# Kernel tuning notes

Hardware: AMD Instinct MI355X
Metric: run time of the kernel (lower is better)

The kernel has to match this reference:

```python
import jax, jax.numpy as jnp
import numpy as np

B = 256      # graph pairs
N = 256      # nodes per graph (uniform -> padding is a reshape)
DEG = 16     # avg degree
D = 32       # one_hot_dim
F1, F2, F3 = 128, 64, 64
T = 16       # tensor_neurons
BINS = 16
BOT = 16     # bottle_neck_neurons


def setup_inputs() -> dict:
    key = jax.random.key(0)
    ks = jax.random.split(key, 24)
    NT = B * N            # total nodes per side
    NE = B * N * DEG      # total directed edges per side
    x_q = jax.random.normal(ks[0], (NT, D), jnp.float32)
    x_c = jax.random.normal(ks[1], (NT, D), jnp.float32)
    edge_q = jax.random.randint(ks[2], (2, NE), 0, NT, jnp.int32)
    edge_c = jax.random.randint(ks[3], (2, NE), 0, NT, jnp.int32)
    qgraph_sizes = jnp.full((B,), N, jnp.int32)
    cgraph_sizes = jnp.full((B,), N, jnp.int32)

    def glorot(k, shape):
        fan = sum(shape[-2:]) if len(shape) >= 2 else shape[0] * 2
        return jax.random.uniform(k, shape, jnp.float32, -1.0, 1.0) * np.sqrt(6.0 / fan)

    params = dict(
        W1=glorot(ks[4], (D, F1)), b1=jnp.zeros((F1,), jnp.float32),
        W2=glorot(ks[5], (F1, F2)), b2=jnp.zeros((F2,), jnp.float32),
        W3=glorot(ks[6], (F2, F3)), b3=jnp.zeros((F3,), jnp.float32),
        attn_w=glorot(ks[7], (F3, F3)),
        ntn_a_w=glorot(ks[8], (T, F3, F3)),
        ntn_b_w=glorot(ks[9], (2 * F3, T)),
        ntn_bias=glorot(ks[10], (T, 1)),
        fc1_w=glorot(ks[11], (T + BINS, BOT)), fc1_b=jnp.zeros((BOT,), jnp.float32),
        fc2_w=glorot(ks[12], (BOT, 1)), fc2_b=jnp.zeros((1,), jnp.float32),
    )
    return dict(x_q=x_q, edge_q=edge_q, x_c=x_c, edge_c=edge_c,
                qgraph_sizes=qgraph_sizes, cgraph_sizes=cgraph_sizes, **params)


def _gcn(x, src, dst, W, b):
    n = x.shape[0]
    h = x @ W
    loop = jnp.arange(n, dtype=src.dtype)
    s = jnp.concatenate([src, loop])
    d = jnp.concatenate([dst, loop])
    deg = jax.ops.segment_sum(jnp.ones(s.shape, h.dtype), d, num_segments=n)
    dinv = jnp.where(deg > 0, jax.lax.rsqrt(jnp.maximum(deg, 1.0)), 0.0)
    coef = (dinv[s] * dinv[d])[:, None]
    return jax.ops.segment_sum(h[s] * coef, d, num_segments=n) + b


def _gnn(x, ei, W1, b1, W2, b2, W3, b3):
    src, dst = ei[0], ei[1]
    h = jax.nn.relu(_gcn(x, src, dst, W1, b1))        # dropout is identity in eval
    h = jax.nn.relu(_gcn(h, src, dst, W2, b2))
    return _gcn(h, src, dst, W3, b3)                  # [B*N, F3]


def _att_pool(q, attn_w, sizes):
    # q: [B, N, F3]
    ctx = jnp.tanh((q.sum(axis=1) @ attn_w) / sizes.astype(q.dtype)[:, None])  # [B, F3]
    sig = jax.nn.sigmoid(jnp.einsum('bnf,bf->bn', q, ctx))                      # [B, N]
    return jnp.einsum('bnf,bn->bf', q, sig)                                     # [B, F3]


def _pair_hist(q, c):
    # per-pair histogram of q @ c^T with BINS bins over each pair's [min, max]
    s = jax.lax.stop_gradient(jnp.einsum('bnf,bmf->bnm', q, c))  # [B, N, N]
    mn = s.min(axis=(1, 2), keepdims=True)
    mx = s.max(axis=(1, 2), keepdims=True)
    idx = jnp.clip(jnp.floor((s - mn) / jnp.maximum(mx - mn, 1e-12) * BINS),
                   0, BINS - 1).astype(jnp.int32)
    gid = (idx + jnp.arange(B, dtype=jnp.int32)[:, None, None] * BINS).reshape(-1)
    h = jax.ops.segment_sum(jnp.ones(gid.shape, jnp.float32), gid,
                            num_segments=B * BINS).reshape(B, BINS)
    return h / h.sum(axis=1, keepdims=True)


def reference(x_q, edge_q, x_c, edge_c, qgraph_sizes, cgraph_sizes,
              W1, b1, W2, b2, W3, b3, attn_w, ntn_a_w, ntn_b_w, ntn_bias,
              fc1_w, fc1_b, fc2_w, fc2_b):
    q = _gnn(x_q, edge_q, W1, b1, W2, b2, W3, b3).reshape(B, N, F3)
    c = _gnn(x_c, edge_c, W1, b1, W2, b2, W3, b3).reshape(B, N, F3)
    e1 = _att_pool(q, attn_w, qgraph_sizes)
    e2 = _att_pool(c, attn_w, cgraph_sizes)
    ntn = (jnp.einsum('bi,tij,bj->bt', e1, ntn_a_w, e2)
           + jnp.concatenate([e1, e2], axis=-1) @ ntn_b_w
           + ntn_bias[:, 0])
    scores = jax.nn.relu(ntn)                                   # [B, T]
    hist = _pair_hist(q, c)                                     # [B, BINS]
    scores = jnp.concatenate([scores, hist], axis=1)
    scores = jax.nn.relu(scores @ fc1_w + fc1_b)
    p = jax.nn.sigmoid(scores @ fc2_w + fc2_b)[:, 0]            # [B]
    ged = -0.5 * (qgraph_sizes + cgraph_sizes).astype(p.dtype) * jnp.log(p)
    return ged
```

## Files before the change

### kernel.cpp

```cpp
#include <hip/hip_runtime.h>
#include <hip/hip_bf16.h>
#include <math.h>

#define BB 256
#define NN 256
#define NT (BB*NN)
#define NT2 (2*NT)
#define NE (NT*16)
#define DD 32
#define F1C 128
#define F2C 64
#define F3C 64
#define TT 16
#define BINS 16

#define NBUCK 256
#define BSHIFT 9
#define BNODES 512
#define BCAP 10240
#define EPB 4096

typedef __attribute__((ext_vector_type(8))) short short8;
typedef __attribute__((ext_vector_type(4))) float f32x4;
typedef __attribute__((ext_vector_type(2))) float f32x2;

__device__ inline float b2f(ushort u) { return __uint_as_float(((uint)u) << 16); }
__device__ inline ushort f2b(float f) {
    uint u = __float_as_uint(f);
    return (ushort)((u + 0x7fffu + ((u >> 16) & 1u)) >> 16);
}
__device__ inline float clamp8(float v) { return fminf(fmaxf(v, -448.0f), 448.0f); }
__device__ inline uchar f2f8(float v) {
    int r = __builtin_amdgcn_cvt_pk_fp8_f32(clamp8(v), 0.0f, 0, false);
    return (uchar)(r & 0xff);
}
__device__ inline void f8x8_acc(uint2 w, float* acc) {
    f32x2 p;
    p = __builtin_amdgcn_cvt_pk_f32_fp8(w.x, false); acc[0] += p.x; acc[1] += p.y;
    p = __builtin_amdgcn_cvt_pk_f32_fp8(w.x, true);  acc[2] += p.x; acc[3] += p.y;
    p = __builtin_amdgcn_cvt_pk_f32_fp8(w.y, false); acc[4] += p.x; acc[5] += p.y;
    p = __builtin_amdgcn_cvt_pk_f32_fp8(w.y, true);  acc[6] += p.x; acc[7] += p.y;
}
__device__ inline uint2 f8x8_pack(const float* v) {
    uint2 r;
    r.x = (uint)__builtin_amdgcn_cvt_pk_fp8_f32(clamp8(v[0]), clamp8(v[1]), 0, false);
    r.x = (uint)__builtin_amdgcn_cvt_pk_fp8_f32(clamp8(v[2]), clamp8(v[3]), (int)r.x, true);
    r.y = (uint)__builtin_amdgcn_cvt_pk_fp8_f32(clamp8(v[4]), clamp8(v[5]), 0, false);
    r.y = (uint)__builtin_amdgcn_cvt_pk_fp8_f32(clamp8(v[6]), clamp8(v[7]), (int)r.y, true);
    return r;
}

__global__ __launch_bounds__(256) void zero_k(int* __restrict__ gcount) {
    gcount[threadIdx.x] = 0;
}

__global__ __launch_bounds__(256) void csr_p1_k(const int* __restrict__ eq, const int* __restrict__ ec,
                                                uint* __restrict__ staged, int* __restrict__ gcount) {
    __shared__ uint s_pk[EPB];
    __shared__ int s_cnt[NBUCK];
    __shared__ int s_off[NBUCK];
    __shared__ int s_base[NBUCK];
    __shared__ int s_gb[NBUCK];
    int t = threadIdx.x;
    bool sideB = blockIdx.x >= 256;
    const int* edge = sideB ? ec : eq;
    int off = sideB ? NT : 0;
    int e0 = (blockIdx.x & 255) * EPB;
    s_cnt[t] = 0;
    __syncthreads();
    uint pk[16]; int bk[16];
#pragma unroll
    for (int j = 0; j < 16; j++) {
        int e = e0 + j * 256 + t;
        int s = edge[e] + off;
        int d = edge[NE + e] + off;
        bk[j] = d >> BSHIFT;
        pk[j] = ((uint)s << BSHIFT) | (uint)(d & (BNODES - 1));
        atomicAdd(&s_cnt[bk[j]], 1);
    }
    __syncthreads();
    s_off[t] = s_cnt[t];
    __syncthreads();
    for (int o = 1; o < NBUCK; o <<= 1) {
        int x = (t >= o) ? s_off[t - o] : 0;
        __syncthreads();
        s_off[t] += x;
        __syncthreads();
    }
    {
        int ex = s_off[t] - s_cnt[t];
        s_base[t] = ex;
        s_off[t] = ex;
        s_gb[t] = atomicAdd(&gcount[t], s_cnt[t]);
    }
    __syncthreads();
#pragma unroll
    for (int j = 0; j < 16; j++) {
        int pos = atomicAdd(&s_off[bk[j]], 1);
        s_pk[pos] = pk[j];
    }
    __syncthreads();
    int w = t >> 6, l = t & 63;
    int bsel = l >> 4, l16 = l & 15;
    for (int pb = w; pb < NBUCK / 4; pb += 4) {
        int b = pb * 4 + bsel;
        int n = s_cnt[b], st = s_base[b], gb = s_gb[b];
        if (gb + n > BCAP) n = max(0, BCAP - gb);
        for (int i = l16; i < n; i += 16)
            staged[b * BCAP + gb + i] = s_pk[st + i];
    }
}

__global__ __launch_bounds__(256) void csr_p2_k(const uint* __restrict__ staged, const int* __restrict__ gcount,
                                                int* __restrict__ rp, int* __restrict__ indeg,
                                                float* __restrict__ dinv, int* __restrict__ ep) {
    int b = blockIdx.x;
    int t = threadIdx.x;
    __shared__ int cnt[BNODES];
    __shared__ int fl[BNODES];
    __shared__ int wsum[256];
    __shared__ int gsc[NBUCK];
    cnt[t] = 0; cnt[t + 256] = 0;
    gsc[t] = min(gcount[t], BCAP);
    __syncthreads();
    for (int off = 1; off < NBUCK; off <<= 1) {
        int x = (t >= off) ? gsc[t - off] : 0;
        __syncthreads();
        gsc[t] += x;
        __syncthreads();
    }
    int gbase = (b == 0) ? 0 : gsc[b - 1];
    int n = min(gcount[b], BCAP);
    const uint* sb = staged + (size_t)b * BCAP;
    int i = t;
    for (; i + 768 < n; i += 1024) {
        uint p0 = sb[i];
        uint p1 = sb[i + 256];
        uint p2 = sb[i + 512];
        uint p3 = sb[i + 768];
        atomicAdd(&cnt[p0 & (BNODES - 1)], 1);
        atomicAdd(&cnt[p1 & (BNODES - 1)], 1);
        atomicAdd(&cnt[p2 & (BNODES - 1)], 1);
        atomicAdd(&cnt[p3 & (BNODES - 1)], 1);
    }
    for (; i < n; i += 256)
        atomicAdd(&cnt[sb[i] & (BNODES - 1)], 1);
    __syncthreads();
    int base2 = t * 2;
    int c0 = cnt[base2], c1 = cnt[base2 + 1];
    int s2 = c0 + c1;
    wsum[t] = s2;
    __syncthreads();
    for (int off = 1; off < 256; off <<= 1) {
        int x = (t >= off) ? wsum[t - off] : 0;
        __syncthreads();
        wsum[t] += x;
        __syncthreads();
    }
    int p = gbase + wsum[t] - s2;
    int v0 = b * BNODES + base2;
    rp[v0] = p;          fl[base2] = p;
    indeg[v0] = c0;      dinv[v0] = rsqrtf((float)(c0 + 1));
    p += c0;
    rp[v0 + 1] = p;      fl[base2 + 1] = p;
    indeg[v0 + 1] = c1;  dinv[v0 + 1] = rsqrtf((float)(c1 + 1));
    __syncthreads();
    i = t;
    for (; i + 768 < n; i += 1024) {
        uint p0 = sb[i];
        uint p1 = sb[i + 256];
        uint p2 = sb[i + 512];
        uint p3 = sb[i + 768];
        ep[atomicAdd(&fl[p0 & (BNODES - 1)], 1)] = (int)(p0 >> BSHIFT);
        ep[atomicAdd(&fl[p1 & (BNODES - 1)], 1)] = (int)(p1 >> BSHIFT);
        ep[atomicAdd(&fl[p2 & (BNODES - 1)], 1)] = (int)(p2 >> BSHIFT);
        ep[atomicAdd(&fl[p3 & (BNODES - 1)], 1)] = (int)(p3 >> BSHIFT);
    }
    for (; i < n; i += 256) {
        uint pk = sb[i];
        ep[atomicAdd(&fl[pk & (BNODES - 1)], 1)] = (int)(pk >> BSHIFT);
    }
}

__global__ __launch_bounds__(256) void cvt2w_k(const float* __restrict__ a, const float* __restrict__ b,
                                               const float* __restrict__ dinv, ushort* __restrict__ out,
                                               const float* __restrict__ W1, const float* __restrict__ W2,
                                               const float* __restrict__ W3, ushort* __restrict__ Wt1,
                                               ushort* __restrict__ Wt2, uchar* __restrict__ Wt3f8) {
    const int NB_X = NT2 * DD / 4 / 256;
    if (blockIdx.x < NB_X) {
        int i = blockIdx.x * 256 + threadIdx.x;
        const int per = NT * DD / 4;
        bool sideB = i >= per;
        const float4* src = (const float4*)(sideB ? b : a);
        float4 v = src[sideB ? i - per : i];
        float dv = dinv[i / (DD / 4)];
        ushort4 o;
        o.x = f2b(v.x * dv); o.y = f2b(v.y * dv); o.z = f2b(v.z * dv); o.w = f2b(v.w * dv);
        ((ushort4*)out)[i] = o;
    } else {
        int i = (blockIdx.x - NB_X) * 256 + threadIdx.x;
        if (i < DD * F1C)  { int k = i / F1C, n = i % F1C; Wt1[n * DD + k]  = f2b(W1[i]); }
        if (i < F1C * F2C) { int k = i / F2C, n = i % F2C; Wt2[n * F1C + k] = f2b(W2[i]); }
        if (i < F2C * F3C) { int k = i / F3C, n = i % F3C; Wt3f8[n * F2C + k] = f2f8(W3[i]); }
    }
}

template<int F, bool BIAS, bool RELU>
__global__ __launch_bounds__(256) void agg_bf_k(const ushort* __restrict__ in, const int* __restrict__ rp,
                                                const int* __restrict__ indeg, const int* __restrict__ ep,
                                                const float* __restrict__ dinv,
                                                const float* __restrict__ bias, ushort* __restrict__ out) {
    constexpr int LPV = F / 8;
    constexpr int VPB = 256 / LPV;
    int g = threadIdx.x / LPV;
    int l = threadIdx.x % LPV;
    int v = blockIdx.x * VPB + g;
    float dv = dinv[v];
    short8 rs = *(const short8*)(in + (size_t)v * F + l * 8);
    float acc[8];
#pragma unroll
    for (int j = 0; j < 8; j++) acc[j] = b2f((ushort)rs[j]);
    int start = rp[v];
    int cnt   = indeg[v];
    int i = 0;
    for (; i + 4 <= cnt; i += 4) {
        int s0 = ep[start + i];
        int s1 = ep[start + i + 1];
        int s2 = ep[start + i + 2];
        int s3 = ep[start + i + 3];
        short8 r0 = *(const short8*)(in + (size_t)s0 * F + l * 8);
        short8 r1 = *(const short8*)(in + (size_t)s1 * F + l * 8);
        short8 r2 = *(const short8*)(in + (size_t)s2 * F + l * 8);
        short8 r3 = *(const short8*)(in + (size_t)s3 * F + l * 8);
#pragma unroll
        for (int j = 0; j < 8; j++) {
            acc[j] += b2f((ushort)r0[j]);
            acc[j] += b2f((ushort)r1[j]);
            acc[j] += b2f((ushort)r2[j]);
            acc[j] += b2f((ushort)r3[j]);
        }
    }
    for (; i < cnt; i++) {
        int s0 = ep[start + i];
        short8 r0 = *(const short8*)(in + (size_t)s0 * F + l * 8);
#pragma unroll
        for (int j = 0; j < 8; j++) acc[j] += b2f((ushort)r0[j]);
    }
    short8 o;
#pragma unroll
    for (int j = 0; j < 8; j++) {
        float x = dv * acc[j];
        if (BIAS) x += bias[l * 8 + j];
        if (RELU) x = fmaxf(x, 0.0f);
        o[j] = (short)f2b(x);
    }
    *(short8*)(out + (size_t)v * F + l * 8) = o;
}

template<bool OUT_BF16, bool BIAS, bool RELU>
__global__ __launch_bounds__(256) void agg_f8_k(const uchar* __restrict__ in, const int* __restrict__ rp,
                                                const int* __restrict__ indeg, const int* __restrict__ ep,
                                                const float* __restrict__ dinv,
                                                const float* __restrict__ bias, void* __restrict__ outp) {
    int g = threadIdx.x >> 3;
    int l = threadIdx.x & 7;
    int v = blockIdx.x * 32 + g;
    float dv = dinv[v];
    float acc[8] = {0, 0, 0, 0, 0, 0, 0, 0};
    f8x8_acc(*(const uint2*)(in + (size_t)v * 64 + l * 8), acc);
    int start = rp[v];
    int cnt   = indeg[v];
    int i = 0;
    for (; i + 8 <= cnt; i += 8) {
        int sx[8];
#pragma unroll
        for (int j = 0; j < 8; j++) sx[j] = ep[start + i + j];
        uint2 gx[8];
#pragma unroll
        for (int j = 0; j < 8; j++) gx[j] = *(const uint2*)(in + (size_t)sx[j] * 64 + l * 8);
#pragma unroll
        for (int j = 0; j < 8; j++) f8x8_acc(gx[j], acc);
    }
    for (; i + 4 <= cnt; i += 4) {
        int s0 = ep[start + i];
        int s1 = ep[start + i + 1];
        int s2 = ep[start + i + 2];
        int s3 = ep[start + i + 3];
        uint2 g0 = *(const uint2*)(in + (size_t)s0 * 64 + l * 8);
        uint2 g1 = *(const uint2*)(in + (size_t)s1 * 64 + l * 8);
        uint2 g2 = *(const uint2*)(in + (size_t)s2 * 64 + l * 8);
        uint2 g3 = *(const uint2*)(in + (size_t)s3 * 64 + l * 8);
        f8x8_acc(g0, acc); f8x8_acc(g1, acc); f8x8_acc(g2, acc); f8x8_acc(g3, acc);
    }
    for (; i < cnt; i++) {
        int s0 = ep[start + i];
        f8x8_acc(*(const uint2*)(in + (size_t)s0 * 64 + l * 8), acc);
    }
#pragma unroll
    for (int j = 0; j < 8; j++) {
        float x = dv * acc[j];
        if (BIAS) x += bias[l * 8 + j];
        if (RELU) x = fmaxf(x, 0.0f);
        acc[j] = x;
    }
    if (OUT_BF16) {
        short8 o;
#pragma unroll
        for (int j = 0; j < 8; j++) o[j] = (short)f2b(acc[j]);
        *(short8*)((ushort*)outp + (size_t)v * 64 + l * 8) = o;
    } else {
        *(uint2*)((uchar*)outp + (size_t)v * 64 + l * 8) = f8x8_pack(acc);
    }
}

__global__ __launch_bounds__(256) void gemm12_k(const ushort* __restrict__ xa,
                                                const ushort* __restrict__ Wt1,
                                                const float* __restrict__ b1,
                                                const ushort* __restrict__ Wt2,
                                                const float* __restrict__ dinv,
                                                uchar* __restrict__ h8a) {
    __shared__ ushort s_h1[128][136];
    int w = threadIdx.x >> 6, lane = threadIdx.x & 63;
    int r16 = lane & 15, quad = lane >> 4, koff = quad * 8;
    size_t rows0 = (size_t)blockIdx.x * 128;

    short8 af1[2];
#pragma unroll
    for (int mt = 0; mt < 2; mt++)
        af1[mt] = *(const short8*)(xa + (rows0 + (w * 2 + mt) * 16 + r16) * 32 + koff);
#pragma unroll
    for (int nt = 0; nt < 8; nt++) {
        short8 bfr = *(const short8*)(Wt1 + (size_t)(nt * 16 + r16) * 32 + koff);
        f32x4 acc[2] = {{0.f,0.f,0.f,0.f},{0.f,0.f,0.f,0.f}};
        acc[0] = __builtin_amdgcn_mfma_f32_16x16x32_bf16(af1[0], bfr, acc[0], 0, 0, 0);
        acc[1] = __builtin_amdgcn_mfma_f32_16x16x32_bf16(af1[1], bfr, acc[1], 0, 0, 0);
        int col = nt * 16 + r16;
        float bc = b1[col];
#pragma unroll
        for (int mt = 0; mt < 2; mt++)
#pragma unroll
            for (int r = 0; r < 4; r++) {
                int rl = (w * 2 + mt) * 16 + quad * 4 + r;
                s_h1[rl][col] = f2b(fmaxf(acc[mt][r] + bc, 0.0f));
            }
    }
    __syncthreads();

    short8 af2[4][2];
#pragma unroll
    for (int kc = 0; kc < 4; kc++)
#pragma unroll
        for (int mt = 0; mt < 2; mt++)
            af2[kc][mt] = *(const short8*)&s_h1[(w * 2 + mt) * 16 + r16][kc * 32 + koff];
    float dvr[2][4];
#pragma unroll
    for (int mt = 0; mt < 2; mt++)
#pragma unroll
        for (int r = 0; r < 4; r++)
            dvr[mt][r] = dinv[rows0 + (w * 2 + mt) * 16 + quad * 4 + r];
#pragma unroll
    for (int nt = 0; nt < 4; nt++) {
        f32x4 acc[2] = {{0.f,0.f,0.f,0.f},{0.f,0.f,0.f,0.f}};
#pragma unroll
        for (int kc = 0; kc < 4; kc++) {
            short8 bfr = *(const short8*)(Wt2 + (size_t)(nt * 16 + r16) * 128 + kc * 32 + koff);
            acc[0] = __builtin_amdgcn_mfma_f32_16x16x32_bf16(af2[kc][0], bfr, acc[0], 0, 0, 0);
            acc[1] = __builtin_amdgcn_mfma_f32_16x16x32_bf16(af2[kc][1], bfr, acc[1], 0, 0, 0);
        }
#pragma unroll
        for (int mt = 0; mt < 2; mt++)
#pragma unroll
            for (int r = 0; r < 4; r++) {
                size_t row = rows0 + (w * 2 + mt) * 16 + quad * 4 + r;
                int col = nt * 16 + r16;
                h8a[row * 64 + col] = f2f8(acc[mt][r] * dvr[mt][r]);
            }
    }
}

__global__ __launch_bounds__(256) void gemm_f8_k(const uchar* __restrict__ A8,
                                                 const uchar* __restrict__ Wt8,
                                                 const float* __restrict__ dinv,
                                                 uchar* __restrict__ out8) {
    int w = threadIdx.x >> 6, lane = threadIdx.x & 63;
    int r16 = lane & 15, koff = (lane >> 4) * 8;
    size_t rows0 = (size_t)blockIdx.x * 128;

    long af[2][2];
#pragma unroll
    for (int kc = 0; kc < 2; kc++)
#pragma unroll
        for (int mt = 0; mt < 2; mt++)
            af[kc][mt] = *(const long*)(A8 + (rows0 + (w * 2 + mt) * 16 + r16) * 64 + kc * 32 + koff);

    float dvr[2][4];
#pragma unroll
    for (int mt = 0; mt < 2; mt++)
#pragma unroll
        for (int r = 0; r < 4; r++)
            dvr[mt][r] = dinv[rows0 + (w * 2 + mt) * 16 + (lane >> 4) * 4 + r];

#pragma unroll
    for (int nt = 0; nt < 4; nt++) {
        f32x4 acc[2] = {{0.f,0.f,0.f,0.f},{0.f,0.f,0.f,0.f}};
#pragma unroll
        for (int kc = 0; kc < 2; kc++) {
            long b = *(const long*)(Wt8 + (size_t)(nt * 16 + r16) * 64 + kc * 32 + koff);
            acc[0] = __builtin_amdgcn_mfma_f32_16x16x32_fp8_fp8(af[kc][0], b, acc[0], 0, 0, 0);
            acc[1] = __builtin_amdgcn_mfma_f32_16x16x32_fp8_fp8(af[kc][1], b, acc[1], 0, 0, 0);
        }
#pragma unroll
        for (int mt = 0; mt < 2; mt++) {
#pragma unroll
            for (int r = 0; r < 4; r++) {
                size_t row = rows0 + (w * 2 + mt) * 16 + (lane >> 4) * 4 + r;
                int col = nt * 16 + (lane & 15);
                out8[row * 64 + col] = f2f8(acc[mt][r] * dvr[mt][r]);
            }
        }
    }
}

__global__ __launch_bounds__(256) void pool_hist_k(const ushort* __restrict__ fin,
                                                   const int* __restrict__ qsz, const int* __restrict__ csz,
                                                   const float* __restrict__ attn_w,
                                                   float* __restrict__ e_out, float* __restrict__ histp) {
    __shared__ float smemf[17472];
    int t = threadIdx.x;
    if (blockIdx.x < 512) {
        int b = blockIdx.x & 255;
        bool is_c = blockIdx.x >= BB;
        const ushort* emb = fin + (size_t)blockIdx.x * NN * F3C;
        float size = (float)((is_c ? csz : qsz)[b]);
        float* eo = e_out + (is_c ? BB * F3C : 0) + b * F3C;
        float (*s_emb)[F3C + 1] = (float(*)[F3C + 1])smemf;
        float* s_red = smemf + 256 * 65;
        float* s_sq  = s_red + 256;
        float* s_ctx = s_sq + 64;
        float* s_sig = s_ctx + 64;
        int f = t & 63;
        int w = t >> 6;
#pragma unroll
        for (int it = 0; it < 8; it++) {
            int idx = it * 2048 + t * 8;
            int row = idx >> 6, f0 = idx & 63;
            short8 v = *(const short8*)(emb + idx);
#pragma unroll
            for (int j = 0; j < 8; j++) s_emb[row][f0 + j] = b2f((ushort)v[j]);
        }
        __syncthreads();
        float psum = 0.0f;
#pragma unroll 8
        for (int i2 = 0; i2 < 64; i2++) psum += s_emb[w * 64 + i2][f];
        s_red[w * 64 + f] = psum;
        __syncthreads();
        if (w == 0) {
            s_sq[f] = s_red[f] + s_red[64 + f] + s_red[128 + f] + s_red[192 + f];
            float acc = 0.0f;
            for (int k = 0; k < 64; k++) acc += s_sq[k] * attn_w[k * 64 + f];
            s_ctx[f] = tanhf(acc / size);
        }
        __syncthreads();
        {
            float acc = 0.0f;
#pragma unroll 8
            for (int k = 0; k < 64; k++) acc += s_emb[t][k] * s_ctx[k];
            s_sig[t] = 1.0f / (1.0f + expf(-acc));
        }
        __syncthreads();
        float eacc = 0.0f;
#pragma unroll 8
        for (int i = 0; i < 64; i++) {
            int n = w * 64 + i;
            eacc += s_sig[n] * s_emb[n][f];
        }
        s_red[w * 64 + f] = eacc;
        __syncthreads();
        if (w == 0) eo[f] = s_red[f] + s_red[64 + f] + s_red[128 + f] + s_red[192 + f];
    } else {
        int b = blockIdx.x - 512;
        const ushort* qb = fin + (size_t)b * NN * 64;
        const ushort* cb = fin + (size_t)(NT + b * NN) * 64;
        int lane = t & 63;
        int w = t >> 6;
        int r16 = lane & 15, koff = (lane >> 4) * 8;
        ushort (*cb_s)[72] = (ushort(*)[72])smemf;
        int* h = (int*)(smemf + 9216);
        int* hp = h + 16 * 256;
        float* smn = (float*)(hp + 256);
        float* smx = smn + 4;
        float* s_sc = smx + 4;

#pragma unroll
        for (int it = 0; it < 8; it++) {
            int idx = it * 2048 + t * 8;
            int row = idx >> 6, f0 = idx & 63;
            *(short8*)&cb_s[row][f0] = *(const short8*)(cb + idx);
        }
        short8 a[4][2];
#pragma unroll
        for (int i = 0; i < 4; i++) {
            int row = (w * 4 + i) * 16 + r16;
#pragma unroll
            for (int kk = 0; kk < 2; kk++)
                a[i][kk] = *(const short8*)(qb + row * 64 + kk * 32 + koff);
        }
        __syncthreads();
        float mn = 1e30f, mx = -1e30f;
        for (int mt = 0; mt < 16; mt++) {
            int crow = mt * 16 + r16;
            short8 b0 = *(const short8*)&cb_s[crow][koff];
            short8 b1 = *(const short8*)&cb_s[crow][32 + koff];
#pragma unroll
            for (int i = 0; i < 4; i++) {
                f32x4 acc = {0.0f, 0.0f, 0.0f, 0.0f};
                acc = __builtin_amdgcn_mfma_f32_16x16x32_bf16(a[i][0], b0, acc, 0, 0, 0);
                acc = __builtin_amdgcn_mfma_f32_16x16x32_bf16(a[i][1], b1, acc, 0, 0, 0);
                mn = fminf(mn, fminf(fminf(acc[0], acc[1]), fminf(acc[2], acc[3])));
                mx = fmaxf(mx, fmaxf(fmaxf(acc[0], acc[1]), fmaxf(acc[2], acc[3])));
            }
        }
        for (int off = 32; off; off >>= 1) {
            mn = fminf(mn, __shfl_xor(mn, off, 64));
            mx = fmaxf(mx, __shfl_xor(mx, off, 64));
        }
        if (lane == 0) { smn[w] = mn; smx[w] = mx; }
        __syncthreads();
        if (t == 0) {
            float m0 = fminf(fminf(smn[0], smn[1]), fminf(smn[2], smn[3]));
            float m1 = fmaxf(fmaxf(smx[0], smx[1]), fmaxf(smx[2], smx[3]));
            s_sc[0] = m0;
            s_sc[1] = 16.0f / fmaxf(m1 - m0, 1e-12f);
        }
#pragma unroll
        for (int i = 0; i < 16; i++) h[i * 256 + t] = 0;
        __syncthreads();
        float bmn = s_sc[0], bscale = s_sc[1];
        for (int mt = 0; mt < 16; mt++) {
            int crow = mt * 16 + r16;
            short8 b0 = *(const short8*)&cb_s[crow][koff];
            short8 b1 = *(const short8*)&cb_s[crow][32 + koff];
#pragma unroll
            for (int i = 0; i < 4; i++) {
                f32x4 acc = {0.0f, 0.0f, 0.0f, 0.0f};
                acc = __builtin_amdgcn_mfma_f32_16x16x32_bf16(a[i][0], b0, acc, 0, 0, 0);
                acc = __builtin_amdgcn_mfma_f32_16x16x32_bf16(a[i][1], b1, acc, 0, 0, 0);
#pragma unroll
                for (int r = 0; r < 4; r++) {
                    int bin = (int)floorf((acc[r] - bmn) * bscale);
                    bin = min(max(bin, 0), 15);
                    h[bin * 256 + t] += 1;
                }
            }
        }
        __syncthreads();
        int bb = t >> 4, part = t & 15;
        int sum = 0;
#pragma unroll
        for (int j = 0; j < 16; j++) sum += h[bb * 256 + part * 16 + j];
        hp[bb * 16 + part] = sum;
        __syncthreads();
        if (t < 16) {
            int s = 0;
#pragma unroll
            for (int j = 0; j < 16; j++) s += hp[t * 16 + j];
            histp[b * 16 + t] = (float)s;
        }
    }
}

__global__ __launch_bounds__(256) void ntn_final_k(const float* __restrict__ e, const float* __restrict__ A,
                                                   const float* __restrict__ bw, const float* __restrict__ bias,
                                                   const float* __restrict__ histp,
                                                   const float* __restrict__ fc1w, const float* __restrict__ fc1b,
                                                   const float* __restrict__ fc2w, const float* __restrict__ fc2b,
                                                   const int* __restrict__ qsz, const int* __restrict__ csz,
                                                   float* __restrict__ out) {
    int b = blockIdx.x;
    int t = threadIdx.x;
    __shared__ float s_e1[64], s_e2[64];
    __shared__ float s_ntn[16];
    __shared__ float s_s[32];
    __shared__ float s_a[16];
    if (t < 64) s_e1[t] = e[b * 64 + t];
    else if (t < 128) s_e2[t - 64] = e[BB * 64 + b * 64 + (t - 64)];
    if (t < 16) s_ntn[t] = 0.0f;
    __syncthreads();
#pragma unroll
    for (int r = 0; r < 4; r++) {
        int idx = t + r * 256;
        int tt = idx >> 6, i = idx & 63;
        const float* Ar = A + (size_t)idx * 64;
        float acc = 0.0f;
        for (int j = 0; j < 64; j++) acc += Ar[j] * s_e2[j];
        atomicAdd(&s_ntn[tt], s_e1[i] * acc);
    }
    __syncthreads();
    if (t < 16) {
        float acc = s_ntn[t] + bias[t];
        for (int k = 0; k < 64; k++) acc += s_e1[k] * bw[k * 16 + t];
        for (int k = 0; k < 64; k++) acc += s_e2[k] * bw[(64 + k) * 16 + t];
        s_s[t] = fmaxf(acc, 0.0f);
        s_s[16 + t] = histp[b * 16 + t] * (1.0f / 65536.0f);
    }
    __syncthreads();
    if (t < 16) {
        float a = fc1b[t];
        for (int k = 0; k < 32; k++) a += s_s[k] * fc1w[k * 16 + t];
        s_a[t] = fmaxf(a, 0.0f);
    }
    __syncthreads();
    if (t == 0) {
        float z = fc2b[0];
        for (int j = 0; j < 16; j++) z += s_a[j] * fc2w[j];
        float nz = -z;
        float sp = (nz > 20.0f) ? nz : log1pf(expf(nz));
        out[b] = 0.5f * (float)(qsz[b] + csz[b]) * sp;
    }
}

extern "C" void kernel_launch(void* const* d_in, const int* in_sizes, int n_in,
                              void* d_out, int out_size, void* d_ws, size_t ws_size,
                              hipStream_t stream) {
    const float* x_q    = (const float*)d_in[0];
    const int*   edge_q = (const int*)d_in[1];
    const float* x_c    = (const float*)d_in[2];
    const int*   edge_c = (const int*)d_in[3];
    const int*   qsz    = (const int*)d_in[4];
    const int*   csz    = (const int*)d_in[5];
    const float* W1 = (const float*)d_in[6];
    const float* b1 = (const float*)d_in[7];
    const float* W2 = (const float*)d_in[8];
    const float* b2 = (const float*)d_in[9];
    const float* W3 = (const float*)d_in[10];
    const float* b3 = (const float*)d_in[11];
    const float* attn_w  = (const float*)d_in[12];
    const float* ntn_a   = (const float*)d_in[13];
    const float* ntn_b   = (const float*)d_in[14];
    const float* ntn_bias= (const float*)d_in[15];
    const float* fc1w = (const float*)d_in[16];
    const float* fc1b = (const float*)d_in[17];
    const float* fc2w = (const float*)d_in[18];
    const float* fc2b = (const float*)d_in[19];
    float* out = (float*)d_out;

    char* w = (char*)d_ws;
    auto alloc = [&](size_t bytes) -> void* {
        void* p = (void*)w;
        w += (bytes + 255) & ~(size_t)255;
        return p;
    };
    int*    rp     = (int*)alloc((size_t)NT2 * 4);
    int*    indeg  = (int*)alloc((size_t)NT2 * 4);
    float*  dinv   = (float*)alloc((size_t)NT2 * 4);
    int*    gcount = (int*)alloc(NBUCK * 4);
    uint*   staged = (uint*)alloc((size_t)NBUCK * BCAP * 4);
    int*    ep     = (int*)alloc((size_t)2 * NE * 4);
    ushort* xb     = (ushort*)alloc((size_t)NT2 * 32 * 2);
    ushort* xa     = (ushort*)alloc((size_t)NT2 * 32 * 2);
    uchar*  h8a    = (uchar*)alloc((size_t)NT2 * 64);
    uchar*  h8b    = (uchar*)alloc((size_t)NT2 * 64);
    ushort* fin    = (ushort*)alloc((size_t)NT2 * 64 * 2);
    ushort* Wt1    = (ushort*)alloc((size_t)DD * F1C * 2);
    ushort* Wt2    = (ushort*)alloc((size_t)F1C * F2C * 2);
    uchar*  Wt3f8  = (uchar*)alloc((size_t)F2C * F3C);
    float*  e12    = (float*)alloc(2 * BB * 64 * 4);
    float*  histp  = (float*)alloc(256 * 16 * 4);

    zero_k<<<1, 256, 0, stream>>>(gcount);
    csr_p1_k<<<512, 256, 0, stream>>>(edge_q, edge_c, staged, gcount);
    csr_p2_k<<<NBUCK, 256, 0, stream>>>(staged, gcount, rp, indeg, dinv, ep);

    cvt2w_k<<<NT2 * 32 / 4 / 256 + 64, 256, 0, stream>>>(x_q, x_c, dinv, xb,
                                                         W1, W2, W3, Wt1, Wt2, Wt3f8);

    agg_bf_k<32, false, false><<<NT2 / 64, 256, 0, stream>>>(xb, rp, indeg, ep, dinv, nullptr, xa);
    gemm12_k<<<NT2 / 128, 256, 0, stream>>>(xa, Wt1, b1, Wt2, dinv, h8a);
    agg_f8_k<false, true, true><<<NT2 / 32, 256, 0, stream>>>(h8a, rp, indeg, ep, dinv, b2, h8b);
    gemm_f8_k<<<NT2 / 128, 256, 0, stream>>>(h8b, Wt3f8, dinv, h8a);
    agg_f8_k<true, true, false><<<NT2 / 32, 256, 0, stream>>>(h8a, rp, indeg, ep, dinv, b3, fin);

    pool_hist_k<<<768, 256, 0, stream>>>(fin, qsz, csz, attn_w, e12, histp);
    ntn_final_k<<<BB, 256, 0, stream>>>(e12, ntn_a, ntn_b, ntn_bias, histp,
                                        fc1w, fc1b, fc2w, fc2b, qsz, csz, out);
}
```

Before: 285.5 us.

## Fuse neighbor aggregation into GEMM kernels and merge CSR pass with input conversion

Aggregation for layers 1 and 2 now runs inside the same kernel as the following dense transform, with the aggregated rows staged in LDS instead of written to and reread from global memory. Input conversion no longer waits on dinv, so it is folded into the CSR bucketing kernel and source-side dinv is applied per edge during the gather. The NTN kernel replaces LDS atomics with vectorized loads and a wave shuffle reduction. Together these cut launches and intermediate traffic, at the cost of extra per-edge dinv loads and fewer, heavier blocks for the gather phase.

```diff
diff --git a/kernel.cpp b/kernel.cpp
--- a/kernel.cpp
+++ b/kernel.cpp
@@ -54,60 +54,81 @@
     gcount[threadIdx.x] = 0;
 }
 
-__global__ __launch_bounds__(256) void csr_p1_k(const int* __restrict__ eq, const int* __restrict__ ec,
-                                                uint* __restrict__ staged, int* __restrict__ gcount) {
-    __shared__ uint s_pk[EPB];
-    __shared__ int s_cnt[NBUCK];
-    __shared__ int s_off[NBUCK];
-    __shared__ int s_base[NBUCK];
-    __shared__ int s_gb[NBUCK];
+__global__ __launch_bounds__(256) void p1cvt_k(const int* __restrict__ eq, const int* __restrict__ ec,
+                                               uint* __restrict__ staged, int* __restrict__ gcount,
+                                               const float* __restrict__ a, const float* __restrict__ b,
+                                               ushort* __restrict__ out,
+                                               const float* __restrict__ W1, const float* __restrict__ W2,
+                                               const float* __restrict__ W3, ushort* __restrict__ Wt1,
+                                               ushort* __restrict__ Wt2, uchar* __restrict__ Wt3f8) {
     int t = threadIdx.x;
-    bool sideB = blockIdx.x >= 256;
-    const int* edge = sideB ? ec : eq;
-    int off = sideB ? NT : 0;
-    int e0 = (blockIdx.x & 255) * EPB;
-    s_cnt[t] = 0;
-    __syncthreads();
-    uint pk[16]; int bk[16];
-#pragma unroll
-    for (int j = 0; j < 16; j++) {
-        int e = e0 + j * 256 + t;
-        int s = edge[e] + off;
-        int d = edge[NE + e] + off;
-        bk[j] = d >> BSHIFT;
-        pk[j] = ((uint)s << BSHIFT) | (uint)(d & (BNODES - 1));
-        atomicAdd(&s_cnt[bk[j]], 1);
-    }
-    __syncthreads();
-    s_off[t] = s_cnt[t];
-    __syncthreads();
-    for (int o = 1; o < NBUCK; o <<= 1) {
-        int x = (t >= o) ? s_off[t - o] : 0;
-        __syncthreads();
-        s_off[t] += x;
-        __syncthreads();
-    }
-    {
-        int ex = s_off[t] - s_cnt[t];
-        s_base[t] = ex;
-        s_off[t] = ex;
-        s_gb[t] = atomicAdd(&gcount[t], s_cnt[t]);
-    }
-    __syncthreads();
-#pragma unroll
-    for (int j = 0; j < 16; j++) {
-        int pos = atomicAdd(&s_off[bk[j]], 1);
-        s_pk[pos] = pk[j];
-    }
-    __syncthreads();
-    int w = t >> 6, l = t & 63;
-    int bsel = l >> 4, l16 = l & 15;
-    for (int pb = w; pb < NBUCK / 4; pb += 4) {
-        int b = pb * 4 + bsel;
-        int n = s_cnt[b], st = s_base[b], gb = s_gb[b];
-        if (gb + n > BCAP) n = max(0, BCAP - gb);
-        for (int i = l16; i < n; i += 16)
-            staged[b * BCAP + gb + i] = s_pk[st + i];
+    if (blockIdx.x < 512) {
+        __shared__ uint s_pk[EPB];
+        __shared__ int s_cnt[NBUCK];
+        __shared__ int s_off[NBUCK];
+        __shared__ int s_base[NBUCK];
+        __shared__ int s_gb[NBUCK];
+        bool sideB = blockIdx.x >= 256;
+        const int* edge = sideB ? ec : eq;
+        int off = sideB ? NT : 0;
+        int e0 = (blockIdx.x & 255) * EPB;
+        s_cnt[t] = 0;
+        __syncthreads();
+        uint pk[16]; int bk[16];
+#pragma unroll
+        for (int j = 0; j < 16; j++) {
+            int e = e0 + j * 256 + t;
+            int s = edge[e] + off;
+            int d = edge[NE + e] + off;
+            bk[j] = d >> BSHIFT;
+            pk[j] = ((uint)s << BSHIFT) | (uint)(d & (BNODES - 1));
+            atomicAdd(&s_cnt[bk[j]], 1);
+        }
+        __syncthreads();
+        s_off[t] = s_cnt[t];
+        __syncthreads();
+        for (int o = 1; o < NBUCK; o <<= 1) {
+            int x = (t >= o) ? s_off[t - o] : 0;
+            __syncthreads();
+            s_off[t] += x;
+            __syncthreads();
+        }
+        {
+            int ex = s_off[t] - s_cnt[t];
+            s_base[t] = ex;
+            s_off[t] = ex;
+            s_gb[t] = atomicAdd(&gcount[t], s_cnt[t]);
+        }
+        __syncthreads();
+#pragma unroll
+        for (int j = 0; j < 16; j++) {
+            int pos = atomicAdd(&s_off[bk[j]], 1);
+            s_pk[pos] = pk[j];
+        }
+        __syncthreads();
+        int w = t >> 6, l = t & 63;
+        int bsel = l >> 4, l16 = l & 15;
+        for (int pb = w; pb < NBUCK / 4; pb += 4) {
+            int bkt = pb * 4 + bsel;
+            int n = s_cnt[bkt], st = s_base[bkt], gb = s_gb[bkt];
+            if (gb + n > BCAP) n = max(0, BCAP - gb);
+            for (int i = l16; i < n; i += 16)
+                staged[bkt * BCAP + gb + i] = s_pk[st + i];
+        }
+    } else if (blockIdx.x < 512 + NT2 * DD / 4 / 256) {
+        int i = (blockIdx.x - 512) * 256 + t;
+        const int per = NT * DD / 4;
+        bool sideB = i >= per;
+        const float4* src = (const float4*)(sideB ? b : a);
+        float4 v = src[sideB ? i - per : i];
+        ushort4 o;
+        o.x = f2b(v.x); o.y = f2b(v.y); o.z = f2b(v.z); o.w = f2b(v.w);
+        ((ushort4*)out)[i] = o;
+    } else {
+        int i = (blockIdx.x - (512 + NT2 * DD / 4 / 256)) * 256 + t;
+        if (i < DD * F1C)  { int k = i / F1C, n = i % F1C; Wt1[n * DD + k]  = f2b(W1[i]); }
+        if (i < F1C * F2C) { int k = i / F2C, n = i % F2C; Wt2[n * F1C + k] = f2b(W2[i]); }
+        if (i < F2C * F3C) { int k = i / F3C, n = i % F3C; Wt3f8[n * F2C + k] = f2f8(W3[i]); }
     }
 }
 
@@ -182,80 +203,201 @@
     }
 }
 
-__global__ __launch_bounds__(256) void cvt2w_k(const float* __restrict__ a, const float* __restrict__ b,
-                                               const float* __restrict__ dinv, ushort* __restrict__ out,
-                                               const float* __restrict__ W1, const float* __restrict__ W2,
-                                               const float* __restrict__ W3, ushort* __restrict__ Wt1,
-                                               ushort* __restrict__ Wt2, uchar* __restrict__ Wt3f8) {
-    const int NB_X = NT2 * DD / 4 / 256;
-    if (blockIdx.x < NB_X) {
-        int i = blockIdx.x * 256 + threadIdx.x;
-        const int per = NT * DD / 4;
-        bool sideB = i >= per;
-        const float4* src = (const float4*)(sideB ? b : a);
-        float4 v = src[sideB ? i - per : i];
-        float dv = dinv[i / (DD / 4)];
-        ushort4 o;
-        o.x = f2b(v.x * dv); o.y = f2b(v.y * dv); o.z = f2b(v.z * dv); o.w = f2b(v.w * dv);
-        ((ushort4*)out)[i] = o;
-    } else {
-        int i = (blockIdx.x - NB_X) * 256 + threadIdx.x;
-        if (i < DD * F1C)  { int k = i / F1C, n = i % F1C; Wt1[n * DD + k]  = f2b(W1[i]); }
-        if (i < F1C * F2C) { int k = i / F2C, n = i % F2C; Wt2[n * F1C + k] = f2b(W2[i]); }
-        if (i < F2C * F3C) { int k = i / F3C, n = i % F3C; Wt3f8[n * F2C + k] = f2f8(W3[i]); }
-    }
-}
-
-template<int F, bool BIAS, bool RELU>
-__global__ __launch_bounds__(256) void agg_bf_k(const ushort* __restrict__ in, const int* __restrict__ rp,
-                                                const int* __restrict__ indeg, const int* __restrict__ ep,
-                                                const float* __restrict__ dinv,
-                                                const float* __restrict__ bias, ushort* __restrict__ out) {
-    constexpr int LPV = F / 8;
-    constexpr int VPB = 256 / LPV;
-    int g = threadIdx.x / LPV;
-    int l = threadIdx.x % LPV;
-    int v = blockIdx.x * VPB + g;
-    float dv = dinv[v];
-    short8 rs = *(const short8*)(in + (size_t)v * F + l * 8);
-    float acc[8];
-#pragma unroll
-    for (int j = 0; j < 8; j++) acc[j] = b2f((ushort)rs[j]);
-    int start = rp[v];
-    int cnt   = indeg[v];
-    int i = 0;
-    for (; i + 4 <= cnt; i += 4) {
-        int s0 = ep[start + i];
-        int s1 = ep[start + i + 1];
-        int s2 = ep[start + i + 2];
-        int s3 = ep[start + i + 3];
-        short8 r0 = *(const short8*)(in + (size_t)s0 * F + l * 8);
-        short8 r1 = *(const short8*)(in + (size_t)s1 * F + l * 8);
-        short8 r2 = *(const short8*)(in + (size_t)s2 * F + l * 8);
-        short8 r3 = *(const short8*)(in + (size_t)s3 * F + l * 8);
-#pragma unroll
-        for (int j = 0; j < 8; j++) {
-            acc[j] += b2f((ushort)r0[j]);
-            acc[j] += b2f((ushort)r1[j]);
-            acc[j] += b2f((ushort)r2[j]);
-            acc[j] += b2f((ushort)r3[j]);
-        }
-    }
-    for (; i < cnt; i++) {
-        int s0 = ep[start + i];
-        short8 r0 = *(const short8*)(in + (size_t)s0 * F + l * 8);
-#pragma unroll
-        for (int j = 0; j < 8; j++) acc[j] += b2f((ushort)r0[j]);
-    }
-    short8 o;
-#pragma unroll
-    for (int j = 0; j < 8; j++) {
-        float x = dv * acc[j];
-        if (BIAS) x += bias[l * 8 + j];
-        if (RELU) x = fmaxf(x, 0.0f);
-        o[j] = (short)f2b(x);
-    }
-    *(short8*)(out + (size_t)v * F + l * 8) = o;
+__global__ __launch_bounds__(256) void l1_k(const ushort* __restrict__ xb,
+                                            const ushort* __restrict__ Wt1,
+                                            const float* __restrict__ b1,
+                                            const ushort* __restrict__ Wt2,
+                                            const int* __restrict__ rp,
+                                            const int* __restrict__ indeg,
+                                            const int* __restrict__ ep,
+                                            const float* __restrict__ dinv,
+                                            uchar* __restrict__ h8a) {
+    __shared__ ushort s_x[128][40];
+    __shared__ ushort s_h1[128][136];
+    int t = threadIdx.x;
+    size_t rows0 = (size_t)blockIdx.x * 128;
+
+    int gl = t >> 2;
+    int l4 = t & 3;
+#pragma unroll
+    for (int vt = 0; vt < 2; vt++) {
+        int vloc = vt * 64 + gl;
+        int v = (int)rows0 + vloc;
+        float dv = dinv[v];
+        short8 rs = *(const short8*)(xb + (size_t)v * 32 + l4 * 8);
+        float acc[8];
+#pragma unroll
+        for (int j = 0; j < 8; j++) acc[j] = dv * b2f((ushort)rs[j]);
+        int start = rp[v];
+        int cnt   = indeg[v];
+        int i = 0;
+        for (; i + 8 <= cnt; i += 8) {
+            int sx[8];
+#pragma unroll
+            for (int j = 0; j < 8; j++) sx[j] = ep[start + i + j];
+            float ds[8];
+#pragma unroll
+            for (int j = 0; j < 8; j++) ds[j] = dinv[sx[j]];
+            short8 r[8];
+#pragma unroll
+            for (int j = 0; j < 8; j++) r[j] = *(const short8*)(xb + (size_t)sx[j] * 32 + l4 * 8);
+#pragma unroll
+            for (int j = 0; j < 8; j++)
+#pragma unroll
+                for (int k = 0; k < 8; k++) acc[k] += ds[j] * b2f((ushort)r[j][k]);
+        }
+        for (; i < cnt; i++) {
+            int s0 = ep[start + i];
+            float d0 = dinv[s0];
+            short8 r0 = *(const short8*)(xb + (size_t)s0 * 32 + l4 * 8);
+#pragma unroll
+            for (int j = 0; j < 8; j++) acc[j] += d0 * b2f((ushort)r0[j]);
+        }
+        short8 o;
+#pragma unroll
+        for (int j = 0; j < 8; j++) o[j] = (short)f2b(dv * acc[j]);
+        *(short8*)&s_x[vloc][l4 * 8] = o;
+    }
+    __syncthreads();
+
+    int w = t >> 6, lane = t & 63;
+    int r16 = lane & 15, quad = lane >> 4, koff = quad * 8;
+
+    short8 af1[2];
+#pragma unroll
+    for (int mt = 0; mt < 2; mt++)
+        af1[mt] = *(const short8*)&s_x[(w * 2 + mt) * 16 + r16][koff];
+#pragma unroll
+    for (int nt = 0; nt < 8; nt++) {
+        short8 bfr = *(const short8*)(Wt1 + (size_t)(nt * 16 + r16) * 32 + koff);
+        f32x4 acc[2] = {{0.f,0.f,0.f,0.f},{0.f,0.f,0.f,0.f}};
+        acc[0] = __builtin_amdgcn_mfma_f32_16x16x32_bf16(af1[0], bfr, acc[0], 0, 0, 0);
+        acc[1] = __builtin_amdgcn_mfma_f32_16x16x32_bf16(af1[1], bfr, acc[1], 0, 0, 0);
+        int col = nt * 16 + r16;
+        float bc = b1[col];
+#pragma unroll
+        for (int mt = 0; mt < 2; mt++)
+#pragma unroll
+            for (int r = 0; r < 4; r++) {
+                int rl = (w * 2 + mt) * 16 + quad * 4 + r;
+                s_h1[rl][col] = f2b(fmaxf(acc[mt][r] + bc, 0.0f));
+            }
+    }
+    __syncthreads();
+
+    short8 af2[4][2];
+#pragma unroll
+    for (int kc = 0; kc < 4; kc++)
+#pragma unroll
+        for (int mt = 0; mt < 2; mt++)
+            af2[kc][mt] = *(const short8*)&s_h1[(w * 2 + mt) * 16 + r16][kc * 32 + koff];
+    float dvr[2][4];
+#pragma unroll
+    for (int mt = 0; mt < 2; mt++)
+#pragma unroll
+        for (int r = 0; r < 4; r++)
+            dvr[mt][r] = dinv[rows0 + (w * 2 + mt) * 16 + quad * 4 + r];
+#pragma unroll
+    for (int nt = 0; nt < 4; nt++) {
+        f32x4 acc[2] = {{0.f,0.f,0.f,0.f},{0.f,0.f,0.f,0.f}};
+#pragma unroll
+        for (int kc = 0; kc < 4; kc++) {
+            short8 bfr = *(const short8*)(Wt2 + (size_t)(nt * 16 + r16) * 128 + kc * 32 + koff);
+            acc[0] = __builtin_amdgcn_mfma_f32_16x16x32_bf16(af2[kc][0], bfr, acc[0], 0, 0, 0);
+            acc[1] = __builtin_amdgcn_mfma_f32_16x16x32_bf16(af2[kc][1], bfr, acc[1], 0, 0, 0);
+        }
+#pragma unroll
+        for (int mt = 0; mt < 2; mt++)
+#pragma unroll
+            for (int r = 0; r < 4; r++) {
+                size_t row = rows0 + (w * 2 + mt) * 16 + quad * 4 + r;
+                int col = nt * 16 + r16;
+                h8a[row * 64 + col] = f2f8(acc[mt][r] * dvr[mt][r]);
+            }
+    }
+}
+
+__global__ __launch_bounds__(256) void l2_k(const uchar* __restrict__ in,
+                                            const int* __restrict__ rp,
+                                            const int* __restrict__ indeg,
+                                            const int* __restrict__ ep,
+                                            const float* __restrict__ dinv,
+                                            const float* __restrict__ b2,
+                                            const uchar* __restrict__ Wt8,
+                                            uchar* __restrict__ out8) {
+    __shared__ uchar s_a[128][72];
+    int t = threadIdx.x;
+    size_t rows0 = (size_t)blockIdx.x * 128;
+
+    int g8 = t >> 3;
+    int l8 = t & 7;
+#pragma unroll
+    for (int pass = 0; pass < 4; pass++) {
+        int vloc = pass * 32 + g8;
+        int v = (int)rows0 + vloc;
+        float dv = dinv[v];
+        float acc[8] = {0, 0, 0, 0, 0, 0, 0, 0};
+        f8x8_acc(*(const uint2*)(in + (size_t)v * 64 + l8 * 8), acc);
+        int start = rp[v];
+        int cnt   = indeg[v];
+        int i = 0;
+        for (; i + 8 <= cnt; i += 8) {
+            int sx[8];
+#pragma unroll
+            for (int j = 0; j < 8; j++) sx[j] = ep[start + i + j];
+            uint2 gx[8];
+#pragma unroll
+            for (int j = 0; j < 8; j++) gx[j] = *(const uint2*)(in + (size_t)sx[j] * 64 + l8 * 8);
+#pragma unroll
+            for (int j = 0; j < 8; j++) f8x8_acc(gx[j], acc);
+        }
+        for (; i < cnt; i++) {
+            int s0 = ep[start + i];
+            f8x8_acc(*(const uint2*)(in + (size_t)s0 * 64 + l8 * 8), acc);
+        }
+#pragma unroll
+        for (int j = 0; j < 8; j++)
+            acc[j] = fmaxf(dv * acc[j] + b2[l8 * 8 + j], 0.0f);
+        *(uint2*)&s_a[vloc][l8 * 8] = f8x8_pack(acc);
+    }
+    __syncthreads();
+
+    int w = t >> 6, lane = t & 63;
+    int r16 = lane & 15, koff = (lane >> 4) * 8;
+
+    long af[2][2];
+#pragma unroll
+    for (int kc = 0; kc < 2; kc++)
+#pragma unroll
+        for (int mt = 0; mt < 2; mt++)
+            af[kc][mt] = *(const long*)&s_a[(w * 2 + mt) * 16 + r16][kc * 32 + koff];
+
+    float dvr[2][4];
+#pragma unroll
+    for (int mt = 0; mt < 2; mt++)
+#pragma unroll
+        for (int r = 0; r < 4; r++)
+            dvr[mt][r] = dinv[rows0 + (w * 2 + mt) * 16 + (lane >> 4) * 4 + r];
+
+#pragma unroll
+    for (int nt = 0; nt < 4; nt++) {
+        f32x4 acc[2] = {{0.f,0.f,0.f,0.f},{0.f,0.f,0.f,0.f}};
+#pragma unroll
+        for (int kc = 0; kc < 2; kc++) {
+            long b = *(const long*)(Wt8 + (size_t)(nt * 16 + r16) * 64 + kc * 32 + koff);
+            acc[0] = __builtin_amdgcn_mfma_f32_16x16x32_fp8_fp8(af[kc][0], b, acc[0], 0, 0, 0);
+            acc[1] = __builtin_amdgcn_mfma_f32_16x16x32_fp8_fp8(af[kc][1], b, acc[1], 0, 0, 0);
+        }
+#pragma unroll
+        for (int mt = 0; mt < 2; mt++) {
+#pragma unroll
+            for (int r = 0; r < 4; r++) {
+                size_t row = rows0 + (w * 2 + mt) * 16 + (lane >> 4) * 4 + r;
+                int col = nt * 16 + (lane & 15);
+                out8[row * 64 + col] = f2f8(acc[mt][r] * dvr[mt][r]);
+            }
+        }
+    }
 }
 
 template<bool OUT_BF16, bool BIAS, bool RELU>
@@ -311,114 +453,6 @@
         *(short8*)((ushort*)outp + (size_t)v * 64 + l * 8) = o;
     } else {
         *(uint2*)((uchar*)outp + (size_t)v * 64 + l * 8) = f8x8_pack(acc);
-    }
-}
-
-__global__ __launch_bounds__(256) void gemm12_k(const ushort* __restrict__ xa,
-                                                const ushort* __restrict__ Wt1,
-                                                const float* __restrict__ b1,
-                                                const ushort* __restrict__ Wt2,
-                                                const float* __restrict__ dinv,
-                                                uchar* __restrict__ h8a) {
-    __shared__ ushort s_h1[128][136];
-    int w = threadIdx.x >> 6, lane = threadIdx.x & 63;
-    int r16 = lane & 15, quad = lane >> 4, koff = quad * 8;
-    size_t rows0 = (size_t)blockIdx.x * 128;
-
-    short8 af1[2];
-#pragma unroll
-    for (int mt = 0; mt < 2; mt++)
-        af1[mt] = *(const short8*)(xa + (rows0 + (w * 2 + mt) * 16 + r16) * 32 + koff);
-#pragma unroll
-    for (int nt = 0; nt < 8; nt++) {
-        short8 bfr = *(const short8*)(Wt1 + (size_t)(nt * 16 + r16) * 32 + koff);
-        f32x4 acc[2] = {{0.f,0.f,0.f,0.f},{0.f,0.f,0.f,0.f}};
-        acc[0] = __builtin_amdgcn_mfma_f32_16x16x32_bf16(af1[0], bfr, acc[0], 0, 0, 0);
-        acc[1] = __builtin_amdgcn_mfma_f32_16x16x32_bf16(af1[1], bfr, acc[1], 0, 0, 0);
-        int col = nt * 16 + r16;
-        float bc = b1[col];
-#pragma unroll
-        for (int mt = 0; mt < 2; mt++)
-#pragma unroll
-            for (int r = 0; r < 4; r++) {
-                int rl = (w * 2 + mt) * 16 + quad * 4 + r;
-                s_h1[rl][col] = f2b(fmaxf(acc[mt][r] + bc, 0.0f));
-            }
-    }
-    __syncthreads();
-
-    short8 af2[4][2];
-#pragma unroll
-    for (int kc = 0; kc < 4; kc++)
-#pragma unroll
-        for (int mt = 0; mt < 2; mt++)
-            af2[kc][mt] = *(const short8*)&s_h1[(w * 2 + mt) * 16 + r16][kc * 32 + koff];
-    float dvr[2][4];
-#pragma unroll
-    for (int mt = 0; mt < 2; mt++)
-#pragma unroll
-        for (int r = 0; r < 4; r++)
-            dvr[mt][r] = dinv[rows0 + (w * 2 + mt) * 16 + quad * 4 + r];
-#pragma unroll
-    for (int nt = 0; nt < 4; nt++) {
-        f32x4 acc[2] = {{0.f,0.f,0.f,0.f},{0.f,0.f,0.f,0.f}};
-#pragma unroll
-        for (int kc = 0; kc < 4; kc++) {
-            short8 bfr = *(const short8*)(Wt2 + (size_t)(nt * 16 + r16) * 128 + kc * 32 + koff);
-            acc[0] = __builtin_amdgcn_mfma_f32_16x16x32_bf16(af2[kc][0], bfr, acc[0], 0, 0, 0);
-            acc[1] = __builtin_amdgcn_mfma_f32_16x16x32_bf16(af2[kc][1], bfr, acc[1], 0, 0, 0);
-        }
-#pragma unroll
-        for (int mt = 0; mt < 2; mt++)
-#pragma unroll
-            for (int r = 0; r < 4; r++) {
-                size_t row = rows0 + (w * 2 + mt) * 16 + quad * 4 + r;
-                int col = nt * 16 + r16;
-                h8a[row * 64 + col] = f2f8(acc[mt][r] * dvr[mt][r]);
-            }
-    }
-}
-
-__global__ __launch_bounds__(256) void gemm_f8_k(const uchar* __restrict__ A8,
-                                                 const uchar* __restrict__ Wt8,
-                                                 const float* __restrict__ dinv,
-                                                 uchar* __restrict__ out8) {
-    int w = threadIdx.x >> 6, lane = threadIdx.x & 63;
-    int r16 = lane & 15, koff = (lane >> 4) * 8;
-    size_t rows0 = (size_t)blockIdx.x * 128;
-
-    long af[2][2];
-#pragma unroll
-    for (int kc = 0; kc < 2; kc++)
-#pragma unroll
-        for (int mt = 0; mt < 2; mt++)
-            af[kc][mt] = *(const long*)(A8 + (rows0 + (w * 2 + mt) * 16 + r16) * 64 + kc * 32 + koff);
-
-    float dvr[2][4];
-#pragma unroll
-    for (int mt = 0; mt < 2; mt++)
-#pragma unroll
-        for (int r = 0; r < 4; r++)
-            dvr[mt][r] = dinv[rows0 + (w * 2 + mt) * 16 + (lane >> 4) * 4 + r];
-
-#pragma unroll
-    for (int nt = 0; nt < 4; nt++) {
-        f32x4 acc[2] = {{0.f,0.f,0.f,0.f},{0.f,0.f,0.f,0.f}};
-#pragma unroll
-        for (int kc = 0; kc < 2; kc++) {
-            long b = *(const long*)(Wt8 + (size_t)(nt * 16 + r16) * 64 + kc * 32 + koff);
-            acc[0] = __builtin_amdgcn_mfma_f32_16x16x32_fp8_fp8(af[kc][0], b, acc[0], 0, 0, 0);
-            acc[1] = __builtin_amdgcn_mfma_f32_16x16x32_fp8_fp8(af[kc][1], b, acc[1], 0, 0, 0);
-        }
-#pragma unroll
-        for (int mt = 0; mt < 2; mt++) {
-#pragma unroll
-            for (int r = 0; r < 4; r++) {
-                size_t row = rows0 + (w * 2 + mt) * 16 + (lane >> 4) * 4 + r;
-                int col = nt * 16 + (lane & 15);
-                out8[row * 64 + col] = f2f8(acc[mt][r] * dvr[mt][r]);
-            }
-        }
     }
 }
 
@@ -579,22 +613,28 @@
                                                    float* __restrict__ out) {
     int b = blockIdx.x;
     int t = threadIdx.x;
+    int lane = t & 63, w = t >> 6;
     __shared__ float s_e1[64], s_e2[64];
     __shared__ float s_ntn[16];
     __shared__ float s_s[32];
     __shared__ float s_a[16];
     if (t < 64) s_e1[t] = e[b * 64 + t];
     else if (t < 128) s_e2[t - 64] = e[BB * 64 + b * 64 + (t - 64)];
-    if (t < 16) s_ntn[t] = 0.0f;
     __syncthreads();
 #pragma unroll
     for (int r = 0; r < 4; r++) {
         int idx = t + r * 256;
-        int tt = idx >> 6, i = idx & 63;
-        const float* Ar = A + (size_t)idx * 64;
+        const float4* Ar = (const float4*)(A + (size_t)idx * 64);
         float acc = 0.0f;
-        for (int j = 0; j < 64; j++) acc += Ar[j] * s_e2[j];
-        atomicAdd(&s_ntn[tt], s_e1[i] * acc);
+#pragma unroll
+        for (int j = 0; j < 16; j++) {
+            float4 a4 = Ar[j];
+            acc += a4.x * s_e2[4 * j] + a4.y * s_e2[4 * j + 1]
+                 + a4.z * s_e2[4 * j + 2] + a4.w * s_e2[4 * j + 3];
+        }
+        float p = s_e1[lane] * acc;
+        for (int off = 32; off; off >>= 1) p += __shfl_xor(p, off, 64);
+        if (lane == 0) s_ntn[w + 4 * r] = p;
     }
     __syncthreads();
     if (t < 16) {
@@ -658,7 +698,6 @@
     uint*   staged = (uint*)alloc((size_t)NBUCK * BCAP * 4);
     int*    ep     = (int*)alloc((size_t)2 * NE * 4);
     ushort* xb     = (ushort*)alloc((size_t)NT2 * 32 * 2);
-    ushort* xa     = (ushort*)alloc((size_t)NT2 * 32 * 2);
     uchar*  h8a    = (uchar*)alloc((size_t)NT2 * 64);
     uchar*  h8b    = (uchar*)alloc((size_t)NT2 * 64);
     ushort* fin    = (ushort*)alloc((size_t)NT2 * 64 * 2);
@@ -669,17 +708,13 @@
     float*  histp  = (float*)alloc(256 * 16 * 4);
 
     zero_k<<<1, 256, 0, stream>>>(gcount);
-    csr_p1_k<<<512, 256, 0, stream>>>(edge_q, edge_c, staged, gcount);
+    p1cvt_k<<<512 + NT2 * DD / 4 / 256 + 32, 256, 0, stream>>>(
+        edge_q, edge_c, staged, gcount, x_q, x_c, xb, W1, W2, W3, Wt1, Wt2, Wt3f8);
     csr_p2_k<<<NBUCK, 256, 0, stream>>>(staged, gcount, rp, indeg, dinv, ep);
 
-    cvt2w_k<<<NT2 * 32 / 4 / 256 + 64, 256, 0, stream>>>(x_q, x_c, dinv, xb,
-                                                         W1, W2, W3, Wt1, Wt2, Wt3f8);
-
-    agg_bf_k<32, false, false><<<NT2 / 64, 256, 0, stream>>>(xb, rp, indeg, ep, dinv, nullptr, xa);
-    gemm12_k<<<NT2 / 128, 256, 0, stream>>>(xa, Wt1, b1, Wt2, dinv, h8a);
-    agg_f8_k<false, true, true><<<NT2 / 32, 256, 0, stream>>>(h8a, rp, indeg, ep, dinv, b2, h8b);
-    gemm_f8_k<<<NT2 / 128, 256, 0, stream>>>(h8b, Wt3f8, dinv, h8a);
-    agg_f8_k<true, true, false><<<NT2 / 32, 256, 0, stream>>>(h8a, rp, indeg, ep, dinv, b3, fin);
+    l1_k<<<NT2 / 128, 256, 0, stream>>>(xb, Wt1, b1, Wt2, rp, indeg, ep, dinv, h8a);
+    l2_k<<<NT2 / 128, 256, 0, stream>>>(h8a, rp, indeg, ep, dinv, b2, Wt3f8, h8b);
+    agg_f8_k<true, true, false><<<NT2 / 32, 256, 0, stream>>>(h8b, rp, indeg, ep, dinv, b3, fin);
 
     pool_hist_k<<<768, 256, 0, stream>>>(fin, qsz, csz, attn_w, e12, histp);
     ntn_final_k<<<BB, 256, 0, stream>>>(e12, ntn_a, ntn_b, ntn_bias, histp,
```

Measured after the change: 297.0 us. 4.1% more time.
